# Kernel optimization log

Measured on AMD Instinct MI355X. Metric: run time of the kernel, lower is better.

## Reference

```python
import jax, jax.numpy as jnp
import numpy as np
from functools import partial

ALPHA = 0.5
GAMMA = 0.01
BIG = 1e8  # boundary init, matches compute_softdtw (exp(-BIG/gamma)==0)


def pairwise_sq(x, y):
    # x: [N, d], y: [M, d] -> squared euclidean distances [N, M], clamped at 0
    xn = jnp.sum(x * x, axis=1)[:, None]
    yn = jnp.sum(y * y, axis=1)[None, :]
    d = xn + yn - 2.0 * (x @ y.T)
    return jnp.clip(d, 0.0, None)


def softdtw(D, gamma):
    # soft-DTW DP: V[i,j] = D[i-1,j-1] + softmin(V[i,j-1], V[i-1,j-1], V[i-1,j])
    # scan over rows; inner scan over columns (sequential dependence on V[i,j-1])
    N, M = D.shape

    def row_step(prev_row, d_row):
        # prev_row: V[i-1, 0..M]  (length M+1)
        def col_step(v_left, inp):
            d, v_diag, v_up = inp
            r = jnp.stack([v_left, v_diag, v_up]) * (-1.0 / gamma)
            v = d - gamma * jax.nn.logsumexp(r)  # stable soft-min
            return v, v

        _, row_vals = jax.lax.scan(
            col_step,
            jnp.asarray(BIG, D.dtype),                 # V[i, 0]
            (d_row, prev_row[:-1], prev_row[1:]),      # D[i-1,j-1], V[i-1,j-1], V[i-1,j]
        )
        new_row = jnp.concatenate([jnp.full((1,), BIG, D.dtype), row_vals])
        return new_row, None

    init_row = jnp.concatenate(
        [jnp.zeros((1,), D.dtype), jnp.full((M,), BIG, D.dtype)]
    )  # V[0, :] row with V[0,0]=0
    last_row, _ = jax.lax.scan(row_step, init_row, D)
    return last_row[-1]  # V[N, M]


def dilate_loss(y_pred, y_true, alpha=ALPHA, gamma=GAMMA):
    B, N = y_pred.shape[0], y_pred.shape[1]
    t = y_true.reshape(B, -1, 1)
    o = y_pred.reshape(B, -1, 1)
    D = jax.vmap(pairwise_sq)(t, o)  # [B, N, N]

    sd = partial(softdtw, gamma=gamma)
    # shape term: mean soft-DTW value over batch (SoftDTWBatch)
    loss_shape = jnp.mean(jax.vmap(sd)(D))
    # temporal term: E = d softDTW / d D (soft path), mean over batch (PathDTWBatch)
    path = jnp.mean(jax.vmap(jax.grad(sd))(D), axis=0)  # [N, N]
    idx = jnp.arange(1, N + 1, dtype=y_pred.dtype)
    omega = (idx[:, None] - idx[None, :]) ** 2  # pairwise_distances(range(1,N+1))
    loss_temporal = jnp.sum(path * omega) / (N * N)

    return alpha * loss_shape + (1.0 - alpha) * loss_temporal


def setup_inputs() -> dict:
    key = jax.random.key(0)
    k1, k2 = jax.random.split(key)
    B, N = 64, 256
    y_pred = jax.random.normal(k1, (B, N, 1), dtype=jnp.float32)
    y_true = jax.random.normal(k2, (B, N, 1), dtype=jnp.float32)
    return {"y_pred": y_pred, "y_true": y_true}


def reference(y_pred, y_true):
    return dilate_loss(y_pred, y_true)
```

## Files before the change

kernel.cpp:

```cpp
#include <hip/hip_runtime.h>

#define BATCH 64
#define NN 256
#define CSC   144.26950408889634f
#define RCSC  0.0069314718055994531f
#define BIGS  1.4426950408889634e10f


__device__ __forceinline__ float shr1(float x, float old) {
    return __int_as_float(__builtin_amdgcn_update_dpp(
        __float_as_int(old), __float_as_int(x), 0x138, 0xF, 0xF, false));
}

#define ITER(J, OINJ) {                                              \
    float sA = shr1(A, rdcA);                                        \
    float sU = shr1(U, rdcU);                                        \
    oc = shr1(oc, OINJ);                                             \
    rdcA = rdnA; rdcU = rdnU;                                        \
    float2 rr = ringr[((J) + 9) & 15];             \
    rdnA = rr.x; rdnU = rr.y;                                        \
    float m  = fminf(fminf(A, psA), sA);                             \
    float el = __builtin_amdgcn_exp2f(m - A);                        \
    float ed = __builtin_amdgcn_exp2f(m - psA);                      \
    float eu = __builtin_amdgcn_exp2f(m - sA);                       \
    float s  = el + ed + eu;                                         \
    float x  = T - oc;                                               \
    float nv = fmaf(CSC * x, x, m - __builtin_amdgcn_logf(s));       \
    float num = fmaf(el, U, fmaf(ed, psU, eu * sU));                 \
    float nt  = fmaf(num, __builtin_amdgcn_rcpf(s), dr * dr);        \
    if (l63) ringw[(J)] = make_float2(nv, nt);                       \
    psA = sA; psU = sU; A = nv; U = nt; dr -= 1.0f;                  \
}

__global__ __launch_bounds__(256) void dilate_fused(
    const float* __restrict__ y_pred,
    const float* __restrict__ y_true,
    float* __restrict__ out)
{
    const int b   = blockIdx.x;
    const int tid = threadIdx.x;
    const int w   = tid >> 6;
    const int l   = tid & 63;
    const bool l63 = (l == 63);

    __shared__ float  o_lds[1088];
    __shared__ float2 ring[5][16];

    const float4 z4 = make_float4(0.f, 0.f, 0.f, 0.f);
    if (tid < 128) ((float4*)o_lds)[tid] = z4;
    if (tid >= 128 && tid < 208) ((float4*)o_lds)[tid + 64] = z4;
    if (tid < 64) ((float4*)(o_lds + 512))[tid] =
        ((const float4*)(y_pred + b * NN))[tid];
    if (tid < 80) ((float2*)ring)[tid] = make_float2(BIGS, 0.f);

    const float T = y_true[b * NN + tid];
    __syncthreads();

    float A = BIGS, U = 0.f;
    float psA = (tid == 0) ? 0.f : BIGS;
    float psU = 0.f;
    float oc = 0.f;
    float dr = (float)(2 * tid + 8 * w);
    float rdcA = BIGS, rdcU = 0.f, rdnA = BIGS, rdnU = 0.f;

    float2* ringw = ring[w];
    const float2* ringr = ring[(w == 0) ? 4 : (w - 1)];
    const float4* o4 = ((const float4*)o_lds) + (128 - 18 * w);

    float4 fA = o4[0], fB = o4[1], fC = o4[2], fD = o4[3]; o4 += 4;

    #pragma unroll 1
    for (int blk = 0; blk < 33; ++blk) {
        float4 gA = o4[0], gB = o4[1], gC = o4[2], gD = o4[3]; o4 += 4;
        ITER(0,  fA.x) ITER(1,  fA.y) ITER(2,  fA.z) ITER(3,  fA.w)
        __syncthreads();
        ITER(4,  fB.x) ITER(5,  fB.y) ITER(6,  fB.z) ITER(7,  fB.w)
        __syncthreads();
        ITER(8,  fC.x) ITER(9,  fC.y) ITER(10, fC.z) ITER(11, fC.w)
        __syncthreads();
        ITER(12, fD.x) ITER(13, fD.y) ITER(14, fD.z) ITER(15, fD.w)
        __syncthreads();
        fA = gA; fB = gB; fC = gC; fD = gD;
    }
    ITER(0, fA.x) ITER(1, fA.y) ITER(2, fA.z) ITER(3, fA.w)
    ITER(4, fB.x) ITER(5, fB.y) ITER(6, fB.z)

    if (tid == 255) {
        float loss = 0.5f * (A * RCSC) * (1.0f / BATCH)
                   + 0.5f * U * (1.0f / ((float)BATCH * (float)(NN * NN)));
        atomicAdd(out, loss);
    }
}

extern "C" void kernel_launch(void* const* d_in, const int* in_sizes, int n_in,
                              void* d_out, int out_size, void* d_ws, size_t ws_size,
                              hipStream_t stream)
{
    const float* y_pred = (const float*)d_in[0];
    const float* y_true = (const float*)d_in[1];
    hipMemsetAsync(d_out, 0, sizeof(float), stream);
    dilate_fused<<<BATCH, 256, 0, stream>>>(y_pred, y_true, (float*)d_out);
}
```

Measured before the change: 97.85 us.

## Pack two batch elements per 512-thread block with separate LDS regions

Each block now processes two independent batch items, 256 threads each, with duplicated LDS buffers and rings, and the grid is halved to 32 blocks. The barriers inside the wavefront pipeline are now shared by eight waves spanning two independent problems. This may reduce per-block launch overhead or change CU packing, but it couples the two problems at every barrier and uses fewer CUs on a chip with many of them.

Result: slower. 117.8 us (+20.4%).

```diff
diff --git a/kernel.cpp b/kernel.cpp
--- a/kernel.cpp
+++ b/kernel.cpp
@@ -32,40 +32,43 @@
     psA = sA; psU = sU; A = nv; U = nt; dr -= 1.0f;                  \
 }
 
-__global__ __launch_bounds__(256) void dilate_fused(
+__global__ __launch_bounds__(512) void dilate_fused(
     const float* __restrict__ y_pred,
     const float* __restrict__ y_true,
     float* __restrict__ out)
 {
-    const int b   = blockIdx.x;
     const int tid = threadIdx.x;
-    const int w   = tid >> 6;
+    const int h   = tid >> 8;
+    const int q   = tid & 255;
+    const int b   = blockIdx.x * 2 + h;
+    const int w   = q >> 6;
     const int l   = tid & 63;
     const bool l63 = (l == 63);
 
-    __shared__ float  o_lds[1088];
-    __shared__ float2 ring[5][16];
+    __shared__ float  o_lds[2][1088];
+    __shared__ float2 ring[2][5][16];
 
+    float* oh = o_lds[h];
     const float4 z4 = make_float4(0.f, 0.f, 0.f, 0.f);
-    if (tid < 128) ((float4*)o_lds)[tid] = z4;
-    if (tid >= 128 && tid < 208) ((float4*)o_lds)[tid + 64] = z4;
-    if (tid < 64) ((float4*)(o_lds + 512))[tid] =
-        ((const float4*)(y_pred + b * NN))[tid];
-    if (tid < 80) ((float2*)ring)[tid] = make_float2(BIGS, 0.f);
+    if (q < 128) ((float4*)oh)[q] = z4;
+    if (q >= 128 && q < 208) ((float4*)oh)[q + 64] = z4;
+    if (q < 64) ((float4*)(oh + 512))[q] =
+        ((const float4*)(y_pred + b * NN))[q];
+    if (q < 80) ((float2*)ring[h])[q] = make_float2(BIGS, 0.f);
 
-    const float T = y_true[b * NN + tid];
+    const float T = y_true[b * NN + q];
     __syncthreads();
 
     float A = BIGS, U = 0.f;
-    float psA = (tid == 0) ? 0.f : BIGS;
+    float psA = (q == 0) ? 0.f : BIGS;
     float psU = 0.f;
     float oc = 0.f;
-    float dr = (float)(2 * tid + 8 * w);
+    float dr = (float)(2 * q + 8 * w);
     float rdcA = BIGS, rdcU = 0.f, rdnA = BIGS, rdnU = 0.f;
 
-    float2* ringw = ring[w];
-    const float2* ringr = ring[(w == 0) ? 4 : (w - 1)];
-    const float4* o4 = ((const float4*)o_lds) + (128 - 18 * w);
+    float2* ringw = ring[h][w];
+    const float2* ringr = ring[h][(w == 0) ? 4 : (w - 1)];
+    const float4* o4 = ((const float4*)oh) + (128 - 18 * w);
 
     float4 fA = o4[0], fB = o4[1], fC = o4[2], fD = o4[3]; o4 += 4;
 
@@ -85,7 +88,7 @@
     ITER(0, fA.x) ITER(1, fA.y) ITER(2, fA.z) ITER(3, fA.w)
     ITER(4, fB.x) ITER(5, fB.y) ITER(6, fB.z)
 
-    if (tid == 255) {
+    if (q == 255) {
         float loss = 0.5f * (A * RCSC) * (1.0f / BATCH)
                    + 0.5f * U * (1.0f / ((float)BATCH * (float)(NN * NN)));
         atomicAdd(out, loss);
@@ -99,5 +102,5 @@
     const float* y_pred = (const float*)d_in[0];
     const float* y_true = (const float*)d_in[1];
     hipMemsetAsync(d_out, 0, sizeof(float), stream);
-    dilate_fused<<<BATCH, 256, 0, stream>>>(y_pred, y_true, (float*)d_out);
+    dilate_fused<<<BATCH / 2, 512, 0, stream>>>(y_pred, y_true, (float*)d_out);
 }
```

## Compute soft-DTW with one wave per batch, four rows per lane

Applied to the files above, without the earlier changes.

Replaces the four-wave wavefront, which passed boundary values through an LDS ring with barriers every four steps, with a single 64-lane wave in which each lane owns four consecutive rows. The four cells are computed per diagonal step inside registers, and only the lane-to-lane shift carries dependencies. This removes block barriers and LDS ring traffic but lengthens the serial dependency chain per step and reduces active waves per block.

Result: slower. 114.9 us (+17.4%).

```diff
diff --git a/kernel.cpp b/kernel.cpp
--- a/kernel.cpp
+++ b/kernel.cpp
@@ -12,82 +12,78 @@
         __float_as_int(old), __float_as_int(x), 0x138, 0xF, 0xF, false));
 }
 
-#define ITER(J, OINJ) {                                              \
-    float sA = shr1(A, rdcA);                                        \
-    float sU = shr1(U, rdcU);                                        \
-    oc = shr1(oc, OINJ);                                             \
-    rdcA = rdnA; rdcU = rdnU;                                        \
-    float2 rr = ringr[((J) + 9) & 15];             \
-    rdnA = rr.x; rdnU = rr.y;                                        \
-    float m  = fminf(fminf(A, psA), sA);                             \
-    float el = __builtin_amdgcn_exp2f(m - A);                        \
-    float ed = __builtin_amdgcn_exp2f(m - psA);                      \
-    float eu = __builtin_amdgcn_exp2f(m - sA);                       \
+#define CELL(A, U, dA, dU, uA, uU, t, drv) {                         \
+    float m  = fminf(fminf((A), (dA)), (uA));                        \
+    float el = __builtin_amdgcn_exp2f(m - (A));                      \
+    float ed = __builtin_amdgcn_exp2f(m - (dA));                     \
+    float eu = __builtin_amdgcn_exp2f(m - (uA));                     \
     float s  = el + ed + eu;                                         \
-    float x  = T - oc;                                               \
+    float x  = (t) - oc;                                             \
     float nv = fmaf(CSC * x, x, m - __builtin_amdgcn_logf(s));       \
-    float num = fmaf(el, U, fmaf(ed, psU, eu * sU));                 \
-    float nt  = fmaf(num, __builtin_amdgcn_rcpf(s), dr * dr);        \
-    if (l63) ringw[(J)] = make_float2(nv, nt);                       \
-    psA = sA; psU = sU; A = nv; U = nt; dr -= 1.0f;                  \
+    float num = fmaf(el, (U), fmaf(ed, (dU), eu * (uU)));            \
+    float dv = (drv);                                                \
+    float nt  = fmaf(num, __builtin_amdgcn_rcpf(s), dv * dv);        \
+    (A) = nv; (U) = nt;                                              \
 }
 
-__global__ __launch_bounds__(256) void dilate_fused(
+#define ITER(OINJ) {                                                 \
+    float sA = shr1(A4, BIGS);              \
+    float sU = shr1(U4, 0.f);                                        \
+    oc = shr1(oc, OINJ);                            \
+    float oA1 = A1, oU1 = U1;                                        \
+    CELL(A1, U1, pdA, pdU, sA, sU, T.x, drb)                         \
+    pdA = sA; pdU = sU;                                              \
+    float oA2 = A2, oU2 = U2;                                        \
+    CELL(A2, U2, oA1, oU1, A1, U1, T.y, drb + 1.0f)                  \
+    float oA3 = A3, oU3 = U3;                                        \
+    CELL(A3, U3, oA2, oU2, A2, U2, T.z, drb + 2.0f)                  \
+    CELL(A4, U4, oA3, oU3, A3, U3, T.w, drb + 3.0f)                  \
+    drb -= 1.0f;                                                     \
+}
+
+__global__ __launch_bounds__(64) void dilate_fused(
     const float* __restrict__ y_pred,
     const float* __restrict__ y_true,
     float* __restrict__ out)
 {
-    const int b   = blockIdx.x;
-    const int tid = threadIdx.x;
-    const int w   = tid >> 6;
-    const int l   = tid & 63;
-    const bool l63 = (l == 63);
+    const int b = blockIdx.x;
+    const int l = threadIdx.x;
 
-    __shared__ float  o_lds[1088];
-    __shared__ float2 ring[5][16];
+    __shared__ float o_lds[336];
 
-    const float4 z4 = make_float4(0.f, 0.f, 0.f, 0.f);
-    if (tid < 128) ((float4*)o_lds)[tid] = z4;
-    if (tid >= 128 && tid < 208) ((float4*)o_lds)[tid + 64] = z4;
-    if (tid < 64) ((float4*)(o_lds + 512))[tid] =
-        ((const float4*)(y_pred + b * NN))[tid];
-    if (tid < 80) ((float2*)ring)[tid] = make_float2(BIGS, 0.f);
-
-    const float T = y_true[b * NN + tid];
+    ((float4*)o_lds)[l] = ((const float4*)(y_pred + b * NN))[l];
+    if (l < 20) ((float4*)o_lds)[64 + l] = make_float4(0.f, 0.f, 0.f, 0.f);
     __syncthreads();
 
-    float A = BIGS, U = 0.f;
-    float psA = (tid == 0) ? 0.f : BIGS;
-    float psU = 0.f;
-    float oc = 0.f;
-    float dr = (float)(2 * tid + 8 * w);
-    float rdcA = BIGS, rdcU = 0.f, rdnA = BIGS, rdnU = 0.f;
+    const float4 T = ((const float4*)(y_true + b * NN))[l];
 
-    float2* ringw = ring[w];
-    const float2* ringr = ring[(w == 0) ? 4 : (w - 1)];
-    const float4* o4 = ((const float4*)o_lds) + (128 - 18 * w);
+    float A1 = BIGS, A2 = BIGS, A3 = BIGS, A4 = BIGS;
+    float U1 = 0.f,  U2 = 0.f,  U3 = 0.f,  U4 = 0.f;
+    float pdA = (l == 0) ? 0.f : BIGS;
+    float pdU = 0.f;
+    float oc  = 0.f;
+    float drb = (float)(5 * l);
 
+    const float4* o4 = (const float4*)o_lds;
     float4 fA = o4[0], fB = o4[1], fC = o4[2], fD = o4[3]; o4 += 4;
 
     #pragma unroll 1
-    for (int blk = 0; blk < 33; ++blk) {
+    for (int blk = 0; blk < 19; ++blk) {
         float4 gA = o4[0], gB = o4[1], gC = o4[2], gD = o4[3]; o4 += 4;
-        ITER(0,  fA.x) ITER(1,  fA.y) ITER(2,  fA.z) ITER(3,  fA.w)
-        __syncthreads();
-        ITER(4,  fB.x) ITER(5,  fB.y) ITER(6,  fB.z) ITER(7,  fB.w)
-        __syncthreads();
-        ITER(8,  fC.x) ITER(9,  fC.y) ITER(10, fC.z) ITER(11, fC.w)
-        __syncthreads();
-        ITER(12, fD.x) ITER(13, fD.y) ITER(14, fD.z) ITER(15, fD.w)
-        __syncthreads();
+        ITER(fA.x) ITER(fA.y) ITER(fA.z) ITER(fA.w)
+        ITER(fB.x) ITER(fB.y) ITER(fB.z) ITER(fB.w)
+        ITER(fC.x) ITER(fC.y) ITER(fC.z) ITER(fC.w)
+        ITER(fD.x) ITER(fD.y) ITER(fD.z) ITER(fD.w)
         fA = gA; fB = gB; fC = gC; fD = gD;
     }
-    ITER(0, fA.x) ITER(1, fA.y) ITER(2, fA.z) ITER(3, fA.w)
-    ITER(4, fB.x) ITER(5, fB.y) ITER(6, fB.z)
+    ITER(fA.x) ITER(fA.y) ITER(fA.z) ITER(fA.w)
+    ITER(fB.x) ITER(fB.y) ITER(fB.z) ITER(fB.w)
+    ITER(fC.x) ITER(fC.y) ITER(fC.z) ITER(fC.w)
+    ITER(fD.x) ITER(fD.y) ITER(fD.z)
 
-    if (tid == 255) {
-        float loss = 0.5f * (A * RCSC) * (1.0f / BATCH)
-                   + 0.5f * U * (1.0f / ((float)BATCH * (float)(NN * NN)));
+    if (l == 63) {
+        float loss = 0.5f * (A4 * RCSC) * (1.0f / BATCH)
+                   + 0.5f * U4 * (1.0f / ((float)BATCH * (float)(NN * NN)));
         atomicAdd(out, loss);
     }
 }
@@ -99,5 +95,5 @@
     const float* y_pred = (const float*)d_in[0];
     const float* y_true = (const float*)d_in[1];
     hipMemsetAsync(d_out, 0, sizeof(float), stream);
-    dilate_fused<<<BATCH, 256, 0, stream>>>(y_pred, y_true, (float*)d_out);
+    dilate_fused<<<BATCH, 64, 0, stream>>>(y_pred, y_true, (float*)d_out);
 }
```

## Defer log in soft-DTW recurrence by carrying (exponent, scale) pairs

Applied to the files above, without the earlier changes.

Each DP cell now holds its value as a base-2 exponent plus a linear scale factor, so the per-cell log is dropped and applied only every four iterations (STRIP) and at the end. This takes the transcendental log off the serial anti-diagonal critical path. In exchange the code carries an extra DPP shift, three more multiplies, clamps on the scale and the gradient term, and a wider float4 ring in LDS. The scale clamp [1, 65536] may change numerics on edge cases.

New measurement: 113.0 us. 15.5% more time.

```diff
diff --git a/kernel.cpp b/kernel.cpp
--- a/kernel.cpp
+++ b/kernel.cpp
@@ -13,23 +13,35 @@
 }
 
 #define ITER(J, OINJ) {                                              \
-    float sA = shr1(A, rdcA);                                        \
-    float sU = shr1(U, rdcU);                                        \
+    float ua = shr1(Aa, rdca);                                       \
+    float us = shr1(As, rdcs);                                       \
+    float uU = shr1(UU, rdcu);                                       \
     oc = shr1(oc, OINJ);                                             \
-    rdcA = rdnA; rdcU = rdnU;                                        \
-    float2 rr = ringr[((J) + 9) & 15];             \
-    rdnA = rr.x; rdnU = rr.y;                                        \
-    float m  = fminf(fminf(A, psA), sA);                             \
-    float el = __builtin_amdgcn_exp2f(m - A);                        \
-    float ed = __builtin_amdgcn_exp2f(m - psA);                      \
-    float eu = __builtin_amdgcn_exp2f(m - sA);                       \
+    us = fminf(fmaxf(us, 1.0f), 65536.0f);      \
+    rdca = rdna; rdcs = rdns; rdcu = rdnu;                           \
+    float4 rr = ringr[((J) + 9) & 15];             \
+    rdna = rr.x; rdns = rr.y; rdnu = rr.z;                           \
+    float m  = fminf(fminf(Aa, pda), ua);                            \
+    float xl = __builtin_amdgcn_exp2f(m - Aa);                       \
+    float xd = __builtin_amdgcn_exp2f(m - pda);                      \
+    float xu = __builtin_amdgcn_exp2f(m - ua);                       \
+    float el = As * xl;                                              \
+    float ed = pds * xd;                                             \
+    float eu = us * xu;                                              \
     float s  = el + ed + eu;                                         \
-    float x  = T - oc;                                               \
-    float nv = fmaf(CSC * x, x, m - __builtin_amdgcn_logf(s));       \
-    float num = fmaf(el, U, fmaf(ed, psU, eu * sU));                 \
+    float xo = T - oc;                                               \
+    float na = fmaf(CSC * xo, xo, m);                                \
+    float num = fmaf(el, UU, fmaf(ed, pdU, eu * uU));                \
     float nt  = fmaf(num, __builtin_amdgcn_rcpf(s), dr * dr);        \
-    if (l63) ringw[(J)] = make_float2(nv, nt);                       \
-    psA = sA; psU = sU; A = nv; U = nt; dr -= 1.0f;                  \
+    nt = fminf(nt, 1e30f);                      \
+    if (l63) ringw[(J)] = make_float4(na, s, nt, 0.f);               \
+    pda = ua; pds = us; pdU = uU;                                    \
+    Aa = na; As = s; UU = nt; dr -= 1.0f;                            \
+}
+
+#define STRIP() {                                                    \
+    Aa -= __builtin_amdgcn_logf(As);                                 \
+    As = 1.0f;                                                       \
 }
 
 __global__ __launch_bounds__(256) void dilate_fused(
@@ -44,27 +56,28 @@
     const bool l63 = (l == 63);
 
     __shared__ float  o_lds[1088];
-    __shared__ float2 ring[5][16];
+    __shared__ float4 ring[5][16];
 
     const float4 z4 = make_float4(0.f, 0.f, 0.f, 0.f);
     if (tid < 128) ((float4*)o_lds)[tid] = z4;
     if (tid >= 128 && tid < 208) ((float4*)o_lds)[tid + 64] = z4;
     if (tid < 64) ((float4*)(o_lds + 512))[tid] =
         ((const float4*)(y_pred + b * NN))[tid];
-    if (tid < 80) ((float2*)ring)[tid] = make_float2(BIGS, 0.f);
+    if (tid < 80) ((float4*)ring)[tid] = make_float4(BIGS, 1.f, 0.f, 0.f);
 
     const float T = y_true[b * NN + tid];
     __syncthreads();
 
-    float A = BIGS, U = 0.f;
-    float psA = (tid == 0) ? 0.f : BIGS;
-    float psU = 0.f;
+    float Aa = BIGS, As = 1.f, UU = 0.f;
+    float pda = (tid == 0) ? 0.f : BIGS;
+    float pds = 1.f, pdU = 0.f;
     float oc = 0.f;
     float dr = (float)(2 * tid + 8 * w);
-    float rdcA = BIGS, rdcU = 0.f, rdnA = BIGS, rdnU = 0.f;
+    float rdca = BIGS, rdcs = 1.f, rdcu = 0.f;
+    float rdna = BIGS, rdns = 1.f, rdnu = 0.f;
 
-    float2* ringw = ring[w];
-    const float2* ringr = ring[(w == 0) ? 4 : (w - 1)];
+    float4* ringw = ring[w];
+    const float4* ringr = ring[(w == 0) ? 4 : (w - 1)];
     const float4* o4 = ((const float4*)o_lds) + (128 - 18 * w);
 
     float4 fA = o4[0], fB = o4[1], fC = o4[2], fD = o4[3]; o4 += 4;
@@ -74,20 +87,25 @@
         float4 gA = o4[0], gB = o4[1], gC = o4[2], gD = o4[3]; o4 += 4;
         ITER(0,  fA.x) ITER(1,  fA.y) ITER(2,  fA.z) ITER(3,  fA.w)
         __syncthreads();
+        STRIP()
         ITER(4,  fB.x) ITER(5,  fB.y) ITER(6,  fB.z) ITER(7,  fB.w)
         __syncthreads();
+        STRIP()
         ITER(8,  fC.x) ITER(9,  fC.y) ITER(10, fC.z) ITER(11, fC.w)
         __syncthreads();
+        STRIP()
         ITER(12, fD.x) ITER(13, fD.y) ITER(14, fD.z) ITER(15, fD.w)
         __syncthreads();
+        STRIP()
         fA = gA; fB = gB; fC = gC; fD = gD;
     }
     ITER(0, fA.x) ITER(1, fA.y) ITER(2, fA.z) ITER(3, fA.w)
     ITER(4, fB.x) ITER(5, fB.y) ITER(6, fB.z)
 
     if (tid == 255) {
-        float loss = 0.5f * (A * RCSC) * (1.0f / BATCH)
-                   + 0.5f * U * (1.0f / ((float)BATCH * (float)(NN * NN)));
+        float V = (Aa - __builtin_amdgcn_logf(As)) * RCSC;
+        float loss = 0.5f * V * (1.0f / BATCH)
+                   + 0.5f * UU * (1.0f / ((float)BATCH * (float)(NN * NN)));
         atomicAdd(out, loss);
     }
 }
```
